# Optimization experiments

Hardware: AMD Instinct MI355X
Metric: run time of the kernel (lower is better)

Reference implementation:

```python
import jax, jax.numpy as jnp
import numpy as np

# dims
B, T, N, D, H, MRP = 16, 120, 24, 256, 8, 32
DP = D // H  # per-head depth = 32
NEG = -1e9


def setup_inputs() -> dict:
    key = jax.random.key(0)
    ks = jax.random.split(key, 32)
    g = lambda k, shape: jax.random.normal(k, shape, jnp.float32) * 0.02
    inp = {
        'x': jax.random.normal(ks[0], (B, T, N, D), jnp.float32),
        # causal look-ahead mask: 1 where attention is disallowed
        'mask': jnp.triu(jnp.ones((T, T), jnp.float32), 1),
        # per-joint temporal QKV (distinct Linear per joint, as in the per-joint ModuleList loops)
        'wq_t': g(ks[1], (N, D, D)), 'wk_t': g(ks[2], (N, D, D)), 'wv_t': g(ks[3], (N, D, D)),
        'bq_t': jnp.zeros((N, D), jnp.float32), 'bk_t': jnp.zeros((N, D), jnp.float32), 'bv_t': jnp.zeros((N, D), jnp.float32),
        'wo_t': g(ks[4], (D, D)), 'bo_t': jnp.zeros((D,), jnp.float32),
        # relative position key/value embedding tables [2*MRP+1, depth]
        'rel_key': g(ks[5], (2 * MRP + 1, DP)), 'rel_val': g(ks[6], (2 * MRP + 1, DP)),
        # spatial (across-joint) attention: shared linears
        'wq_s': g(ks[7], (D, D)), 'wk_s': g(ks[8], (D, D)), 'wv_s': g(ks[9], (D, D)), 'wo_s': g(ks[10], (D, D)),
        'bq_s': jnp.zeros((D,), jnp.float32), 'bk_s': jnp.zeros((D,), jnp.float32), 'bv_s': jnp.zeros((D,), jnp.float32), 'bo_s': jnp.zeros((D,), jnp.float32),
        # per-joint pointwise FFN
        'ff1_w': g(ks[11], (N, D, D)), 'ff1_b': jnp.zeros((N, D), jnp.float32),
        'ff2_w': g(ks[12], (N, D, D)), 'ff2_b': jnp.zeros((N, D), jnp.float32),
    }
    return inp


def _forward(x, mask, wq_t, wk_t, wv_t, bq_t, bk_t, bv_t, wo_t, bo_t,
             rel_key, rel_val, wq_s, wk_s, wv_s, wo_s, bq_s, bk_s, bv_s, bo_s,
             ff1_w, ff1_b, ff2_w, ff2_b):
    b, t, n, d = x.shape
    dp = d // H
    scale = 1.0 / jnp.sqrt(jnp.float32(dp))

    def joint_proj(y, w, bias):  # per-joint Linear: [b,t,n,d] x [n,d,e]
        return jnp.einsum('btnd,nde->btne', y, w) + bias

    def heads_t(y):  # -> [b, n, h, t, dp]
        return y.reshape(b, t, n, H, dp).transpose(0, 2, 3, 1, 4)

    # ---- temporal attention (per joint, with relative pos key/val embeddings) ----
    q = heads_t(joint_proj(x, wq_t, bq_t))
    k = heads_t(joint_proj(x, wk_t, bk_t))
    v = heads_t(joint_proj(x, wv_t, bv_t))
    rel_idx = jnp.clip(jnp.arange(t)[None, :] - jnp.arange(t)[:, None], -MRP, MRP) + MRP  # [t,t]
    rk = rel_key[rel_idx]   # [t,t,dp]
    rv = rel_val[rel_idx]   # [t,t,dp]
    logits = jnp.einsum('bnhtd,bnhsd->bnhts', q, k) + jnp.einsum('bnhtd,tsd->bnhts', q, rk)
    logits = logits * scale + mask * NEG
    attn = jax.nn.softmax(logits, axis=-1)
    out = jnp.einsum('bnhts,bnhsd->bnhtd', attn, v) + jnp.einsum('bnhts,tsd->bnhtd', attn, rv)
    out = out.transpose(0, 3, 1, 2, 4).reshape(b, t, n, d)
    t_out = jnp.einsum('btnd,de->btne', out, wo_t) + bo_t

    # ---- spatial attention (across joints at each timestep, shared linears) ----
    def heads_s(y):  # [b,t,n,d] -> [b,t,h,n,dp]
        return y.reshape(b, t, n, H, dp).transpose(0, 1, 3, 2, 4)

    qs = heads_s(jnp.einsum('btnd,de->btne', x, wq_s) + bq_s)
    ks_ = heads_s(jnp.einsum('btnd,de->btne', x, wk_s) + bk_s)
    vs = heads_s(jnp.einsum('btnd,de->btne', x, wv_s) + bv_s)
    s_logits = jnp.einsum('bthnd,bthmd->bthnm', qs, ks_) * scale
    s_attn = jax.nn.softmax(s_logits, axis=-1)
    s_out = jnp.einsum('bthnm,bthmd->bthnd', s_attn, vs)
    s_out = s_out.transpose(0, 1, 3, 2, 4).reshape(b, t, n, d)
    s_out = jnp.einsum('btnd,de->btne', s_out, wo_s) + bo_s

    # ---- parallel combination + residual ----
    y = x + t_out + s_out

    # ---- per-joint pointwise FFN + residual ----
    h = jax.nn.relu(joint_proj(y, ff1_w, ff1_b))
    ffn = joint_proj(h, ff2_w, ff2_b)
    return y + ffn


def reference(x, mask, wq_t, wk_t, wv_t, bq_t, bk_t, bv_t, wo_t, bo_t,
              rel_key, rel_val, wq_s, wk_s, wv_s, wo_s, bq_s, bk_s, bv_s, bo_s,
              ff1_w, ff1_b, ff2_w, ff2_b):
    return _forward(x, mask, wq_t, wk_t, wv_t, bq_t, bk_t, bv_t, wo_t, bo_t,
                    rel_key, rel_val, wq_s, wk_s, wv_s, wo_s, bq_s, bk_s, bv_s, bo_s,
                    ff1_w, ff1_b, ff2_w, ff2_b)
```

## Files before the change

kernel.cpp:

```cpp
#include <hip/hip_runtime.h>

#define B_    16
#define T_    120
#define N_    24
#define D_    256
#define H_    8
#define DP_   32
#define MRP_  32
#define BT_   (B_*T_)
#define M_    (B_*T_*N_)
#define TND   (N_*D_)
#define SCALE_ 0.17677669529663687f

typedef __attribute__((ext_vector_type(8))) short bf16x8;
typedef __attribute__((ext_vector_type(4))) float f32x4;

#define MEMBAR() asm volatile("" ::: "memory")

__device__ inline unsigned short f2bf(float f) {
    union { float f; unsigned u; } v; v.f = f;
    return (unsigned short)((v.u + 0x7FFF + ((v.u >> 16) & 1)) >> 16);
}
__device__ inline float bf2f(unsigned short u) {
    union { unsigned u; float f; } v; v.u = ((unsigned)u) << 16;
    return v.f;
}
__device__ __forceinline__ void gld16(const void* g, void* l) {
    __builtin_amdgcn_global_load_lds(
        (__attribute__((address_space(1))) void*)g,
        (__attribute__((address_space(3))) void*)l, 16, 0, 0);
}

__global__ __launch_bounds__(256) void convw(
    const float* __restrict__ wq_t, const float* __restrict__ wk_t,
    const float* __restrict__ wv_t, const float* __restrict__ wo_t,
    const float* __restrict__ wq_s, const float* __restrict__ wk_s,
    const float* __restrict__ wv_s, const float* __restrict__ wo_s,
    const float* __restrict__ ff1_w, const float* __restrict__ ff2_w,
    unsigned short* __restrict__ Wall)
{
    const int bx = blockIdx.x;
    const int m = bx >> 4, tile = bx & 15;
    const int d0 = (tile >> 2) * 64, e0 = (tile & 3) * 64;
    const float* src;
    if      (m < 24)  src = wq_t + (size_t)m * 65536;
    else if (m < 48)  src = wk_t + (size_t)(m-24) * 65536;
    else if (m < 72)  src = wv_t + (size_t)(m-48) * 65536;
    else if (m == 72) src = wo_t;
    else if (m == 73) src = wq_s;
    else if (m == 74) src = wk_s;
    else if (m == 75) src = wv_s;
    else if (m == 76) src = wo_s;
    else if (m < 101) src = ff1_w + (size_t)(m-77) * 65536;
    else              src = ff2_w + (size_t)(m-101) * 65536;
    unsigned short* dst = Wall + (size_t)m * 65536;

    __shared__ float t[64][65];
    const int tid = threadIdx.x;
#pragma unroll
    for (int i = 0; i < 4; ++i) {
        const int dr = (tid >> 4) + i*16;
        const int e4 = (tid & 15) * 4;
        const float4 v = *(const float4*)(src + (size_t)(d0+dr)*256 + e0 + e4);
        t[dr][e4] = v.x; t[dr][e4+1] = v.y; t[dr][e4+2] = v.z; t[dr][e4+3] = v.w;
    }
    __syncthreads();
#pragma unroll
    for (int i = 0; i < 2; ++i) {
        const int er = (tid >> 3) + i*32;
        const int c8 = (tid & 7) * 8;
        unsigned short tmp[8];
#pragma unroll
        for (int j = 0; j < 8; ++j) tmp[j] = f2bf(t[c8+j][er]);
        *(uint4*)&dst[(size_t)(e0+er)*256 + d0 + c8] = *(uint4*)tmp;
    }
}

__global__ __launch_bounds__(256) void convx(const float* __restrict__ x,
                                             unsigned short* __restrict__ xb)
{
    const size_t i = ((size_t)blockIdx.x*256 + threadIdx.x) * 8;
    const float4 a = *(const float4*)(x + i);
    const float4 b = *(const float4*)(x + i + 4);
    unsigned short tmp[8] = { f2bf(a.x), f2bf(a.y), f2bf(a.z), f2bf(a.w),
                              f2bf(b.x), f2bf(b.y), f2bf(b.z), f2bf(b.w) };
    *(uint4*)(xb + i) = *(uint4*)tmp;
}

__global__ __launch_bounds__(256) void convrel(
    const float* __restrict__ rel_key, const float* __restrict__ rel_val,
    unsigned short* __restrict__ relk_img, unsigned short* __restrict__ relv_img)
{
    const int tid = threadIdx.x;
    for (int i = tid; i < 48*32; i += 256) {
        const int c = i >> 5, d = i & 31;
        relk_img[i] = f2bf(rel_key[c*DP_ + d]);
    }
    for (int i = tid; i < 32*72; i += 256) {
        const int d = i / 72, c = i % 72;
        relv_img[i] = (c < 65) ? f2bf(rel_val[c*DP_ + d]) : (unsigned short)0;
    }
}

template<bool PJ>
__global__ __launch_bounds__(256, 6) void mgemm(
    const unsigned short* __restrict__ A, const unsigned short* __restrict__ Wt,
    const float* __restrict__ bias,
    const float* __restrict__ res1, const unsigned short* __restrict__ resb,
    float* __restrict__ outf, unsigned short* __restrict__ outb, int relu)
{
    __shared__ __align__(16) unsigned short As[2][64*32];
    __shared__ __align__(16) unsigned short Bs[2][64*32];
    const int tid  = threadIdx.x;
    const int wave = tid >> 6, lane = tid & 63;
    const int r16  = lane & 15, q4 = lane >> 4;

    const int qg  = (int)gridDim.x >> 3;
    const int wid = (blockIdx.x & 7) * qg + (blockIdx.x >> 3);
    const int rc  = wid >> 2, ec = wid & 3;

    size_t growbase; int rstride;
    const unsigned short* Wp; const float* bp;
    if (PJ) {
        const int n = rc / 30, tile = rc % 30;
        growbase = (size_t)(tile*64) * N_ + n; rstride = N_;
        Wp = Wt + (size_t)n * 65536; bp = bias + n * 256;
    } else {
        growbase = (size_t)rc * 64; rstride = 1;
        Wp = Wt; bp = bias;
    }
    const unsigned short* Wpe = Wp + (size_t)(ec*64) * 256;
    const int e0 = ec * 64;

    f32x4 acc[4];
#pragma unroll
    for (int i = 0; i < 4; ++i) acc[i] = (f32x4){0.f,0.f,0.f,0.f};

    const int arow = tid >> 2, ach = (tid & 3) * 8;

#define STAGE_(kc_, buf_) do {                                                  \
        const int k0_ = (kc_) * 32;                                             \
        gld16(A + (growbase + (size_t)arow*rstride)*256 + k0_ + ach,            \
              &As[buf_][wave*512]);                                             \
        gld16(Wpe + (size_t)arow*256 + k0_ + ach,                               \
              &Bs[buf_][wave*512]);                                             \
    } while (0)

    STAGE_(0, 0);
    STAGE_(1, 1);

#pragma unroll
    for (int kc = 0; kc < 8; ++kc) {
        const int cur = kc & 1;
        if (kc < 7) { asm volatile("s_waitcnt vmcnt(2)" ::: "memory"); }
        else        { asm volatile("s_waitcnt vmcnt(0)" ::: "memory"); }
        __builtin_amdgcn_sched_barrier(0);
        __builtin_amdgcn_s_barrier();

        const bf16x8 af = *(const bf16x8*)&As[cur][(wave*16 + r16)*32 + q4*8];
        bf16x8 bfr[4];
#pragma unroll
        for (int cs = 0; cs < 4; ++cs) bfr[cs] = *(const bf16x8*)&Bs[cur][(cs*16 + r16)*32 + q4*8];
#pragma unroll
        for (int cs = 0; cs < 4; ++cs)
            acc[cs] = __builtin_amdgcn_mfma_f32_16x16x32_bf16(af, bfr[cs], acc[cs], 0, 0, 0);

        __builtin_amdgcn_s_barrier();
        if (kc + 2 < 8) STAGE_(kc + 2, cur);
    }
#undef STAGE_

#pragma unroll
    for (int cs = 0; cs < 4; ++cs) {
        const int e = e0 + cs*16 + r16;
        const float bb = bp[e];
#pragma unroll
        for (int rg = 0; rg < 4; ++rg) {
            const int lr = wave*16 + q4*4 + rg;
            const size_t off = (growbase + (size_t)lr*rstride)*256 + e;
            float v = acc[cs][rg] + bb;
            if (relu) v = fmaxf(v, 0.f);
            if (res1) v += res1[off];
            if (resb) v += bf2f(resb[off]);
            if (outf) outf[off] = v;
            if (outb) outb[off] = f2bf(v);
        }
    }
}

template<bool PJ>
__global__ __launch_bounds__(256, 6) void mgemm_qkv(
    const unsigned short* __restrict__ A, const unsigned short* __restrict__ Wbase,
    const float* __restrict__ bq, const float* __restrict__ bk2,
    const float* __restrict__ bv,
    unsigned short* __restrict__ oq, unsigned short* __restrict__ ok2,
    unsigned short* __restrict__ ov)
{
    __shared__ __align__(16) unsigned short As[2][64*32];
    __shared__ __align__(16) unsigned short Bs[2][64*32];
    const int tid  = threadIdx.x;
    const int wave = tid >> 6, lane = tid & 63;
    const int r16  = lane & 15, q4 = lane >> 4;

    const int qg  = (int)gridDim.x >> 3;
    const int wid = (blockIdx.x & 7) * qg + (blockIdx.x >> 3);
    const int qkv = wid % 3;
    const int t2  = wid / 3;
    const int rc  = t2 >> 2, ec = t2 & 3;

    size_t growbase; int rstride;
    const unsigned short* Wp; const float* bp;
    if (PJ) {
        const int n = rc / 30, tile = rc % 30;
        growbase = (size_t)(tile*64) * N_ + n; rstride = N_;
        Wp = Wbase + ((size_t)qkv * 24 + n) * 65536;
        bp = (qkv == 0 ? bq : qkv == 1 ? bk2 : bv) + n * 256;
    } else {
        growbase = (size_t)rc * 64; rstride = 1;
        Wp = Wbase + (size_t)qkv * 65536;
        bp = (qkv == 0 ? bq : qkv == 1 ? bk2 : bv);
    }
    unsigned short* outp = (qkv == 0 ? oq : qkv == 1 ? ok2 : ov);
    const unsigned short* Wpe = Wp + (size_t)(ec*64) * 256;
    const int e0 = ec * 64;

    f32x4 acc[4];
#pragma unroll
    for (int i = 0; i < 4; ++i) acc[i] = (f32x4){0.f,0.f,0.f,0.f};

    const int arow = tid >> 2, ach = (tid & 3) * 8;

#define STAGE_(kc_, buf_) do {                                                  \
        const int k0_ = (kc_) * 32;                                             \
        gld16(A + (growbase + (size_t)arow*rstride)*256 + k0_ + ach,            \
              &As[buf_][wave*512]);                                             \
        gld16(Wpe + (size_t)arow*256 + k0_ + ach,                               \
              &Bs[buf_][wave*512]);                                             \
    } while (0)

    STAGE_(0, 0);
    STAGE_(1, 1);

#pragma unroll
    for (int kc = 0; kc < 8; ++kc) {
        const int cur = kc & 1;
        if (kc < 7) { asm volatile("s_waitcnt vmcnt(2)" ::: "memory"); }
        else        { asm volatile("s_waitcnt vmcnt(0)" ::: "memory"); }
        __builtin_amdgcn_sched_barrier(0);
        __builtin_amdgcn_s_barrier();

        const bf16x8 af = *(const bf16x8*)&As[cur][(wave*16 + r16)*32 + q4*8];
        bf16x8 bfr[4];
#pragma unroll
        for (int cs = 0; cs < 4; ++cs) bfr[cs] = *(const bf16x8*)&Bs[cur][(cs*16 + r16)*32 + q4*8];
#pragma unroll
        for (int cs = 0; cs < 4; ++cs)
            acc[cs] = __builtin_amdgcn_mfma_f32_16x16x32_bf16(af, bfr[cs], acc[cs], 0, 0, 0);

        __builtin_amdgcn_s_barrier();
        if (kc + 2 < 8) STAGE_(kc + 2, cur);
    }
#undef STAGE_

#pragma unroll
    for (int cs = 0; cs < 4; ++cs) {
        const int e = e0 + cs*16 + r16;
        const float bb = bp[e];
#pragma unroll
        for (int rg = 0; rg < 4; ++rg) {
            const int lr = wave*16 + q4*4 + rg;
            const size_t off = (growbase + (size_t)lr*rstride)*256 + e;
            outp[off] = f2bf(acc[cs][rg] + bb);
        }
    }
}

__global__ __launch_bounds__(256) void temporal_attn(
    const unsigned short* __restrict__ Q, const unsigned short* __restrict__ K,
    const unsigned short* __restrict__ V,
    const unsigned short* __restrict__ relk_img,
    const unsigned short* __restrict__ relv_img,
    unsigned short* __restrict__ out)
{
    __shared__ __align__(16) unsigned short ksb[128*32];
    __shared__ __align__(16) unsigned short vtb[32*136];
    __shared__ __align__(16) unsigned short rkb[48*32];
    __shared__ __align__(16) unsigned short rvtb[32*72];
    __shared__ __align__(16) unsigned short psb[4][16*136];
    __shared__ __align__(16) unsigned short awb[4][16*72];

    const int tid = threadIdx.x, wave = tid >> 6, lane = tid & 63;
    const int r = lane & 15, q4 = lane >> 4;
    const int wid = ((int)blockIdx.x & 7) * 384 + ((int)blockIdx.x >> 3);
    const int h = wid & 7;
    const int bn = wid >> 3;
    const int n = bn % N_;
    const int b = bn / N_;
    const size_t gb = ((size_t)(b*T_)*N_ + n)*D_ + h*DP_;

    {
        const int row0 = tid >> 2, ch0 = (tid & 3) * 8;
        gld16(K + gb + (size_t)row0*TND + ch0, ksb + (size_t)(wave*64)*8);
        int row1 = (256 + tid) >> 2; if (row1 > 119) row1 = 119;
        const int ch1 = ((256 + tid) & 3) * 8;
        gld16(K + gb + (size_t)row1*TND + ch1, ksb + (size_t)(256 + wave*64)*8);
    }
    bf16x8 aqs[2];
#pragma unroll
    for (int ti = 0; ti < 2; ++ti) {
        int qrow = (wave + ti*4)*16 + r; if (qrow > 119) qrow = 119;
        aqs[ti] = *(const bf16x8*)(Q + gb + (size_t)qrow*TND + q4*8);
    }
#pragma unroll
    for (int i = 0; i < 2; ++i) {
        const int slot = tid + i*256;
        if (slot < 480) {
            const int row = slot >> 2, ch = (slot & 3) * 8;
            union { uint4 u; unsigned short h8[8]; } vv;
            vv.u = *(const uint4*)(V + gb + (size_t)row*TND + ch);
#pragma unroll
            for (int j = 0; j < 8; ++j) vtb[(ch+j)*136 + row] = vv.h8[j];
        }
    }
    {
        const int row = tid >> 3, d2 = (tid & 7) * 2;
        *(unsigned*)&vtb[row*136 + 120 + d2] = 0u;
    }
    {
        const uint4* s1 = (const uint4*)relk_img;
        for (int i = tid; i < 192; i += 256) ((uint4*)rkb)[i] = s1[i];
        const uint4* s2 = (const uint4*)relv_img;
        for (int i = tid; i < 288; i += 256) ((uint4*)rvtb)[i] = s2[i];
    }
    __syncthreads();

    unsigned short* psbw = psb[wave];
    unsigned short* awbw = awb[wave];
    float* qrkp = (float*)psbw;

#pragma unroll
    for (int ti = 0; ti < 2; ++ti) {
        const int qt = wave + ti*4;
        const int t0 = qt * 16;
        const int stmax = ti ? 8 : 4;
        const int kcmax = ti ? 4 : 2;

        const bf16x8 aq = aqs[ti];
        __builtin_amdgcn_s_setprio(1);
        f32x4 lgacc[8];
#pragma unroll
        for (int st = 0; st < 8; ++st) {
            if (st < stmax) {
                const bf16x8 bk = *(const bf16x8*)&ksb[(st*16 + r)*32 + q4*8];
                lgacc[st] = __builtin_amdgcn_mfma_f32_16x16x32_bf16(aq, bk, (f32x4){0.f,0.f,0.f,0.f}, 0, 0, 0);
            }
        }
        f32x4 qr[3];
#pragma unroll
        for (int ck = 0; ck < 3; ++ck) {
            const bf16x8 bk = *(const bf16x8*)&rkb[(ck*16 + r)*32 + q4*8];
            qr[ck] = __builtin_amdgcn_mfma_f32_16x16x32_bf16(aq, bk, (f32x4){0.f,0.f,0.f,0.f}, 0, 0, 0);
        }
        __builtin_amdgcn_s_setprio(0);
#pragma unroll
        for (int ck = 0; ck < 3; ++ck)
#pragma unroll
            for (int rr = 0; rr < 4; ++rr)
                qrkp[(q4*4 + rr)*36 + ck*16 + r] = qr[ck][rr];
        MEMBAR();

        float p[4][8], far_[4];
#pragma unroll
        for (int rr = 0; rr < 4; ++rr) {
            const int row = q4*4 + rr;
            const int ta  = t0 + row;
            float v[8];
#pragma unroll
            for (int kt = 0; kt < 8; ++kt) {
                if (kt < stmax) {
                    const int s   = kt*16 + r;
                    const int idx = ta - s;
                    const int c   = (idx >= 32) ? 0 : (32 - idx);
                    const float qv = qrkp[row*36 + c];
                    v[kt] = (idx >= 0) ? (lgacc[kt][rr] + qv) * SCALE_ : -1e30f;
                }
            }
            float mx = v[0];
#pragma unroll
            for (int kt = 1; kt < 8; ++kt)
                if (kt < stmax) mx = fmaxf(mx, v[kt]);
#pragma unroll
            for (int off = 1; off < 16; off <<= 1) mx = fmaxf(mx, __shfl_xor(mx, off));
            float sum = 0.f;
#pragma unroll
            for (int kt = 0; kt < 8; ++kt)
                if (kt < stmax) { v[kt] = __expf(v[kt] - mx); sum += v[kt]; }
#pragma unroll
            for (int off = 1; off < 16; off <<= 1) sum += __shfl_xor(sum, off);
            const float inv = 1.f / sum;
            float fr = 0.f;
#pragma unroll
            for (int kt = 0; kt < 8; ++kt) {
                if (kt < stmax) {
                    p[rr][kt] = v[kt] * inv;
                    const int s = kt*16 + r;
                    if (ta - s >= 32) fr += p[rr][kt];
                }
            }
#pragma unroll
            for (int off = 1; off < 16; off <<= 1) fr += __shfl_xor(fr, off);
            far_[rr] = fr;
        }
        MEMBAR();

#pragma unroll
        for (int i = 0; i < 9; ++i) ((unsigned*)awbw)[lane + i*64] = 0u;
        MEMBAR();
#pragma unroll
        for (int rr = 0; rr < 4; ++rr) {
            const int row = q4*4 + rr;
            const int ta  = t0 + row;
#pragma unroll
            for (int kt = 0; kt < 8; ++kt) {
                if (kt < stmax) {
                    const int s = kt*16 + r;
                    psbw[row*136 + s] = f2bf(p[rr][kt]);
                    const int idx = ta - s;
                    if (idx >= 0 && idx < 32) awbw[row*72 + 32 - idx] = f2bf(p[rr][kt]);
                }
            }
            if (r == 0) awbw[row*72] = f2bf(far_[rr]);
        }
        MEMBAR();

#pragma unroll
        for (int ct = 0; ct < 2; ++ct) {
            f32x4 acc = {0.f, 0.f, 0.f, 0.f};
            __builtin_amdgcn_s_setprio(1);
#pragma unroll
            for (int kc = 0; kc < 4; ++kc) {
                if (kc < kcmax) {
                    const bf16x8 a  = *(const bf16x8*)&psbw[r*136 + kc*32 + q4*8];
                    const bf16x8 bb = *(const bf16x8*)&vtb[(ct*16 + r)*136 + kc*32 + q4*8];
                    acc = __builtin_amdgcn_mfma_f32_16x16x32_bf16(a, bb, acc, 0, 0, 0);
                }
            }
#pragma unroll
            for (int kc = 0; kc < 2; ++kc) {
                const bf16x8 a  = *(const bf16x8*)&awbw[r*72 + kc*32 + q4*8];
                const bf16x8 bb = *(const bf16x8*)&rvtb[(ct*16 + r)*72 + kc*32 + q4*8];
                acc = __builtin_amdgcn_mfma_f32_16x16x32_bf16(a, bb, acc, 0, 0, 0);
            }
            __builtin_amdgcn_s_setprio(0);
#pragma unroll
            for (int rr = 0; rr < 4; ++rr) {
                const int row = t0 + q4*4 + rr;
                if (row < 120)
                    out[gb + (size_t)row*TND + ct*16 + r] = f2bf(acc[rr]);
            }
        }
        MEMBAR();
    }
}

__global__ __launch_bounds__(512) void spatial_attn(
    const unsigned short* __restrict__ Qs, const unsigned short* __restrict__ Ks,
    const unsigned short* __restrict__ Vs, unsigned short* __restrict__ out)
{
    __shared__ __align__(16) unsigned short vt[256*40];
    __shared__ __align__(16) unsigned short pa[8][32*40];
    const int tid = threadIdx.x, wave = tid >> 6, lane = tid & 63;
    const int r16 = lane & 15, q4 = lane >> 4;
    const int h = wave;
    const size_t base = (size_t)blockIdx.x * N_ * D_;

    bf16x8 kf[2], qf[2];
#pragma unroll
    for (int t = 0; t < 2; ++t) {
        int row = t*16 + r16; if (row > 23) row = 23;
        kf[t] = *(const bf16x8*)(Ks + base + (size_t)row*D_ + h*DP_ + q4*8);
        qf[t] = *(const bf16x8*)(Qs + base + (size_t)row*D_ + h*DP_ + q4*8);
    }

    for (int slot = tid; slot < 768; slot += 512) {
        const int m = slot >> 5, ec = slot & 31;
        union { uint4 u; unsigned short s_[8]; } vv;
        vv.u = *(const uint4*)(Vs + base + (size_t)m*D_ + ec*8);
#pragma unroll
        for (int j = 0; j < 8; ++j) vt[(ec*8 + j)*40 + m] = vv.s_[j];
    }
    for (int z = tid; z < 256*4; z += 512)
        *(unsigned*)&vt[(z >> 2)*40 + 24 + (z & 3)*2] = 0u;
    __syncthreads();

    f32x4 st[2][2];
#pragma unroll
    for (int it = 0; it < 2; ++it)
#pragma unroll
        for (int mt = 0; mt < 2; ++mt)
            st[mt][it] = __builtin_amdgcn_mfma_f32_16x16x32_bf16(
                kf[mt], qf[it], (f32x4){0.f,0.f,0.f,0.f}, 0, 0, 0);

    unsigned short* paw = pa[wave];
#pragma unroll
    for (int it = 0; it < 2; ++it) {
        float v[2][4];
#pragma unroll
        for (int mt = 0; mt < 2; ++mt)
#pragma unroll
            for (int rg = 0; rg < 4; ++rg) {
                const int m = mt*16 + q4*4 + rg;
                v[mt][rg] = (m < 24) ? st[mt][it][rg] * SCALE_ : -1e30f;
            }
        float mx = v[0][0];
#pragma unroll
        for (int mt = 0; mt < 2; ++mt)
#pragma unroll
            for (int rg = 0; rg < 4; ++rg) mx = fmaxf(mx, v[mt][rg]);
        mx = fmaxf(mx, __shfl_xor(mx, 16));
        mx = fmaxf(mx, __shfl_xor(mx, 32));
        float sum = 0.f;
#pragma unroll
        for (int mt = 0; mt < 2; ++mt)
#pragma unroll
            for (int rg = 0; rg < 4; ++rg) { v[mt][rg] = __expf(v[mt][rg] - mx); sum += v[mt][rg]; }
        sum += __shfl_xor(sum, 16);
        sum += __shfl_xor(sum, 32);
        const float inv = 1.f / sum;
#pragma unroll
        for (int mt = 0; mt < 2; ++mt) {
            unsigned short p4[4];
#pragma unroll
            for (int rg = 0; rg < 4; ++rg) p4[rg] = f2bf(v[mt][rg] * inv);
            *(uint2*)&paw[(it*16 + r16)*40 + mt*16 + q4*4] = *(uint2*)p4;
        }
    }
    MEMBAR();

    bf16x8 ap[2], bv[2];
#pragma unroll
    for (int t = 0; t < 2; ++t) {
        ap[t] = *(const bf16x8*)&paw[(t*16 + r16)*40 + q4*8];
        bv[t] = *(const bf16x8*)&vt[(h*DP_ + t*16 + r16)*40 + q4*8];
    }
#pragma unroll
    for (int it = 0; it < 2; ++it)
#pragma unroll
        for (int ct = 0; ct < 2; ++ct) {
            const f32x4 o = __builtin_amdgcn_mfma_f32_16x16x32_bf16(
                ap[it], bv[ct], (f32x4){0.f,0.f,0.f,0.f}, 0, 0, 0);
#pragma unroll
            for (int rg = 0; rg < 4; ++rg) {
                const int i = it*16 + q4*4 + rg;
                if (i < 24)
                    out[base + (size_t)i*D_ + h*DP_ + ct*16 + r16] = f2bf(o[rg]);
            }
        }
}

extern "C" void kernel_launch(void* const* d_in, const int* in_sizes, int n_in,
                              void* d_out, int out_size, void* d_ws, size_t ws_size,
                              hipStream_t stream) {
    const float* x       = (const float*)d_in[0];
    const float* wq_t    = (const float*)d_in[2];
    const float* wk_t    = (const float*)d_in[3];
    const float* wv_t    = (const float*)d_in[4];
    const float* bq_t    = (const float*)d_in[5];
    const float* bk_t    = (const float*)d_in[6];
    const float* bv_t    = (const float*)d_in[7];
    const float* wo_t    = (const float*)d_in[8];
    const float* bo_t    = (const float*)d_in[9];
    const float* rel_key = (const float*)d_in[10];
    const float* rel_val = (const float*)d_in[11];
    const float* wq_s    = (const float*)d_in[12];
    const float* wk_s    = (const float*)d_in[13];
    const float* wv_s    = (const float*)d_in[14];
    const float* wo_s    = (const float*)d_in[15];
    const float* bq_s    = (const float*)d_in[16];
    const float* bk_s    = (const float*)d_in[17];
    const float* bv_s    = (const float*)d_in[18];
    const float* bo_s    = (const float*)d_in[19];
    const float* ff1_w   = (const float*)d_in[20];
    const float* ff1_b   = (const float*)d_in[21];
    const float* ff2_w   = (const float*)d_in[22];
    const float* ff2_b   = (const float*)d_in[23];

    float* out = (float*)d_out;
    unsigned short* outbf = (unsigned short*)d_out;
    unsigned short* ws = (unsigned short*)d_ws;
    const size_t WSZ = (size_t)125 * 65536;
    const size_t SZ  = (size_t)M_ * D_;
    unsigned short* Wall = ws;
    unsigned short* xbf  = Wall + WSZ;
    unsigned short* bufA = xbf + SZ;
    unsigned short* bufB = bufA + SZ;
    unsigned short* bufC = bufB + SZ;
    unsigned short* relk = bufC + SZ;
    unsigned short* relv = relk + 1536;

    const dim3 blk(256);

    convw<<<dim3(125*16), blk, 0, stream>>>(wq_t, wk_t, wv_t, wo_t, wq_s, wk_s, wv_s, wo_s, ff1_w, ff2_w, Wall);
    convx<<<dim3(5760), blk, 0, stream>>>(x, xbf);
    convrel<<<dim3(1), blk, 0, stream>>>(rel_key, rel_val, relk, relv);

    mgemm_qkv<true ><<<dim3(8640), blk, 0, stream>>>(xbf, Wall, bq_t, bk_t, bv_t, bufA, bufB, bufC);
    temporal_attn<<<dim3(B_*N_*H_), blk, 0, stream>>>(bufA, bufB, bufC, relk, relv, bufA);
    mgemm<false><<<dim3(2880), blk, 0, stream>>>(bufA, Wall + 72ull*65536, bo_t, nullptr, nullptr, nullptr, outbf, 0);
    mgemm_qkv<false><<<dim3(8640), blk, 0, stream>>>(xbf, Wall + 73ull*65536, bq_s, bk_s, bv_s, bufB, bufC, bufA);
    spatial_attn<<<dim3(BT_), dim3(512), 0, stream>>>(bufB, bufC, bufA, bufB);
    mgemm<false><<<dim3(2880), blk, 0, stream>>>(bufB, Wall + 76ull*65536, bo_s, x, outbf, nullptr, bufC, 0);
    mgemm<true ><<<dim3(2880), blk, 0, stream>>>(bufC, Wall + 77ull*65536, ff1_b, nullptr, nullptr, nullptr, bufA, 1);
    mgemm<true ><<<dim3(2880), blk, 0, stream>>>(bufA, Wall + 101ull*65536, ff2_b, nullptr, bufC, out, nullptr, 0);
}
```

Measured before the change: 443.0 us.

## Fuse conversion kernels and merge both output projections into one concatenated-K GEMM

```diff
diff --git a/kernel.cpp b/kernel.cpp
--- a/kernel.cpp
+++ b/kernel.cpp
@@ -31,74 +31,69 @@
         (__attribute__((address_space(3))) void*)l, 16, 0, 0);
 }
 
-__global__ __launch_bounds__(256) void convw(
+__global__ __launch_bounds__(256) void convall(
     const float* __restrict__ wq_t, const float* __restrict__ wk_t,
     const float* __restrict__ wv_t, const float* __restrict__ wo_t,
     const float* __restrict__ wq_s, const float* __restrict__ wk_s,
     const float* __restrict__ wv_s, const float* __restrict__ wo_s,
     const float* __restrict__ ff1_w, const float* __restrict__ ff2_w,
-    unsigned short* __restrict__ Wall)
-{
-    const int bx = blockIdx.x;
-    const int m = bx >> 4, tile = bx & 15;
-    const int d0 = (tile >> 2) * 64, e0 = (tile & 3) * 64;
-    const float* src;
-    if      (m < 24)  src = wq_t + (size_t)m * 65536;
-    else if (m < 48)  src = wk_t + (size_t)(m-24) * 65536;
-    else if (m < 72)  src = wv_t + (size_t)(m-48) * 65536;
-    else if (m == 72) src = wo_t;
-    else if (m == 73) src = wq_s;
-    else if (m == 74) src = wk_s;
-    else if (m == 75) src = wv_s;
-    else if (m == 76) src = wo_s;
-    else if (m < 101) src = ff1_w + (size_t)(m-77) * 65536;
-    else              src = ff2_w + (size_t)(m-101) * 65536;
-    unsigned short* dst = Wall + (size_t)m * 65536;
-
-    __shared__ float t[64][65];
-    const int tid = threadIdx.x;
-#pragma unroll
-    for (int i = 0; i < 4; ++i) {
-        const int dr = (tid >> 4) + i*16;
-        const int e4 = (tid & 15) * 4;
-        const float4 v = *(const float4*)(src + (size_t)(d0+dr)*256 + e0 + e4);
-        t[dr][e4] = v.x; t[dr][e4+1] = v.y; t[dr][e4+2] = v.z; t[dr][e4+3] = v.w;
-    }
-    __syncthreads();
-#pragma unroll
-    for (int i = 0; i < 2; ++i) {
-        const int er = (tid >> 3) + i*32;
-        const int c8 = (tid & 7) * 8;
-        unsigned short tmp[8];
-#pragma unroll
-        for (int j = 0; j < 8; ++j) tmp[j] = f2bf(t[c8+j][er]);
-        *(uint4*)&dst[(size_t)(e0+er)*256 + d0 + c8] = *(uint4*)tmp;
-    }
-}
-
-__global__ __launch_bounds__(256) void convx(const float* __restrict__ x,
-                                             unsigned short* __restrict__ xb)
-{
-    const size_t i = ((size_t)blockIdx.x*256 + threadIdx.x) * 8;
-    const float4 a = *(const float4*)(x + i);
-    const float4 b = *(const float4*)(x + i + 4);
-    unsigned short tmp[8] = { f2bf(a.x), f2bf(a.y), f2bf(a.z), f2bf(a.w),
-                              f2bf(b.x), f2bf(b.y), f2bf(b.z), f2bf(b.w) };
-    *(uint4*)(xb + i) = *(uint4*)tmp;
-}
-
-__global__ __launch_bounds__(256) void convrel(
-    const float* __restrict__ rel_key, const float* __restrict__ rel_val,
+    const float* __restrict__ x, const float* __restrict__ rel_key,
+    const float* __restrict__ rel_val,
+    unsigned short* __restrict__ Wall, unsigned short* __restrict__ xb,
     unsigned short* __restrict__ relk_img, unsigned short* __restrict__ relv_img)
 {
-    const int tid = threadIdx.x;
-    for (int i = tid; i < 48*32; i += 256) {
-        const int c = i >> 5, d = i & 31;
-        relk_img[i] = f2bf(rel_key[c*DP_ + d]);
-    }
-    for (int i = tid; i < 32*72; i += 256) {
-        const int d = i / 72, c = i % 72;
-        relv_img[i] = (c < 65) ? f2bf(rel_val[c*DP_ + d]) : (unsigned short)0;
+    __shared__ float t[64][65];
+    const int bx = blockIdx.x, tid = threadIdx.x;
+
+    if (bx < 2000) {
+        const int m = bx >> 4, tile = bx & 15;
+        const int d0 = (tile >> 2) * 64, e0 = (tile & 3) * 64;
+        const float* src;
+        if      (m < 24)  src = wq_t + (size_t)m * 65536;
+        else if (m < 48)  src = wk_t + (size_t)(m-24) * 65536;
+        else if (m < 72)  src = wv_t + (size_t)(m-48) * 65536;
+        else if (m == 72) src = wo_t;
+        else if (m == 73) src = wq_s;
+        else if (m == 74) src = wk_s;
+        else if (m == 75) src = wv_s;
+        else if (m == 76) src = wo_s;
+        else if (m < 101) src = ff1_w + (size_t)(m-77) * 65536;
+        else              src = ff2_w + (size_t)(m-101) * 65536;
+        unsigned short* dst = Wall + (size_t)m * 65536;
+
+#pragma unroll
+        for (int i = 0; i < 4; ++i) {
+            const int dr = (tid >> 4) + i*16;
+            const int e4 = (tid & 15) * 4;
+            const float4 v = *(const float4*)(src + (size_t)(d0+dr)*256 + e0 + e4);
+            t[dr][e4] = v.x; t[dr][e4+1] = v.y; t[dr][e4+2] = v.z; t[dr][e4+3] = v.w;
+        }
+        __syncthreads();
+#pragma unroll
+        for (int i = 0; i < 2; ++i) {
+            const int er = (tid >> 3) + i*32;
+            const int c8 = (tid & 7) * 8;
+            unsigned short tmp[8];
+#pragma unroll
+            for (int j = 0; j < 8; ++j) tmp[j] = f2bf(t[c8+j][er]);
+            *(uint4*)&dst[(size_t)(e0+er)*256 + d0 + c8] = *(uint4*)tmp;
+        }
+    } else if (bx < 7760) {
+        const size_t i = ((size_t)(bx - 2000)*256 + tid) * 8;
+        const float4 a = *(const float4*)(x + i);
+        const float4 b = *(const float4*)(x + i + 4);
+        unsigned short tmp[8] = { f2bf(a.x), f2bf(a.y), f2bf(a.z), f2bf(a.w),
+                                  f2bf(b.x), f2bf(b.y), f2bf(b.z), f2bf(b.w) };
+        *(uint4*)(xb + i) = *(uint4*)tmp;
+    } else {
+        for (int i = tid; i < 48*32; i += 256) {
+            const int c = i >> 5, d = i & 31;
+            relk_img[i] = f2bf(rel_key[c*DP_ + d]);
+        }
+        for (int i = tid; i < 32*72; i += 256) {
+            const int d = i / 72, c = i % 72;
+            relv_img[i] = (c < 65) ? f2bf(rel_val[c*DP_ + d]) : (unsigned short)0;
+        }
     }
 }
 
@@ -271,6 +266,83 @@
             const int lr = wave*16 + q4*4 + rg;
             const size_t off = (growbase + (size_t)lr*rstride)*256 + e;
             outp[off] = f2bf(acc[cs][rg] + bb);
+        }
+    }
+}
+
+__global__ __launch_bounds__(256, 6) void mgemm_wo(
+    const unsigned short* __restrict__ A1, const unsigned short* __restrict__ W1,
+    const unsigned short* __restrict__ A2, const unsigned short* __restrict__ W2,
+    const float* __restrict__ b1, const float* __restrict__ b2,
+    const float* __restrict__ resx, unsigned short* __restrict__ outb)
+{
+    __shared__ __align__(16) unsigned short As[2][64*32];
+    __shared__ __align__(16) unsigned short Bs[2][64*32];
+    const int tid  = threadIdx.x;
+    const int wave = tid >> 6, lane = tid & 63;
+    const int r16  = lane & 15, q4 = lane >> 4;
+
+    const int qg  = (int)gridDim.x >> 3;
+    const int wid = (blockIdx.x & 7) * qg + (blockIdx.x >> 3);
+    const int rc  = wid >> 2, ec = wid & 3;
+
+    const size_t growbase = (size_t)rc * 64;
+    const unsigned short* W1e = W1 + (size_t)(ec*64) * 256;
+    const unsigned short* W2e = W2 + (size_t)(ec*64) * 256;
+    const int e0 = ec * 64;
+
+    f32x4 acc[4];
+#pragma unroll
+    for (int i = 0; i < 4; ++i) acc[i] = (f32x4){0.f,0.f,0.f,0.f};
+
+    const int arow = tid >> 2, ach = (tid & 3) * 8;
+
+#define STG_(Ap_, Wp_, kc_, buf_) do {                                          \
+        const int k0_ = (kc_) * 32;                                             \
+        gld16((Ap_) + (growbase + (size_t)arow)*256 + k0_ + ach,                \
+              &As[buf_][wave*512]);                                             \
+        gld16((Wp_) + (size_t)arow*256 + k0_ + ach,                             \
+              &Bs[buf_][wave*512]);                                             \
+    } while (0)
+
+    STG_(A1, W1e, 0, 0);
+    STG_(A1, W1e, 1, 1);
+
+#pragma unroll
+    for (int s = 0; s < 16; ++s) {
+        const int cur = s & 1;
+        if (s < 15) { asm volatile("s_waitcnt vmcnt(2)" ::: "memory"); }
+        else        { asm volatile("s_waitcnt vmcnt(0)" ::: "memory"); }
+        __builtin_amdgcn_sched_barrier(0);
+        __builtin_amdgcn_s_barrier();
+
+        const bf16x8 af = *(const bf16x8*)&As[cur][(wave*16 + r16)*32 + q4*8];
+        bf16x8 bfr[4];
+#pragma unroll
+        for (int cs = 0; cs < 4; ++cs) bfr[cs] = *(const bf16x8*)&Bs[cur][(cs*16 + r16)*32 + q4*8];
+#pragma unroll
+        for (int cs = 0; cs < 4; ++cs)
+            acc[cs] = __builtin_amdgcn_mfma_f32_16x16x32_bf16(af, bfr[cs], acc[cs], 0, 0, 0);
+
+        __builtin_amdgcn_s_barrier();
+        if (s + 2 < 16) {
+            const int ns = s + 2;
+            const unsigned short* Ap = (ns < 8) ? A1 : A2;
+            const unsigned short* Wp = (ns < 8) ? W1e : W2e;
+            STG_(Ap, Wp, ns & 7, cur);
+        }
+    }
+#undef STG_
+
+#pragma unroll
+    for (int cs = 0; cs < 4; ++cs) {
+        const int e = e0 + cs*16 + r16;
+        const float bb = b1[e] + b2[e];
+#pragma unroll
+        for (int rg = 0; rg < 4; ++rg) {
+            const int lr = wave*16 + q4*4 + rg;
+            const size_t off = (growbase + (size_t)lr)*256 + e;
+            outb[off] = f2bf(acc[cs][rg] + bb + resx[off]);
         }
     }
 }
@@ -600,16 +672,17 @@
 
     const dim3 blk(256);
 
-    convw<<<dim3(125*16), blk, 0, stream>>>(wq_t, wk_t, wv_t, wo_t, wq_s, wk_s, wv_s, wo_s, ff1_w, ff2_w, Wall);
-    convx<<<dim3(5760), blk, 0, stream>>>(x, xbf);
-    convrel<<<dim3(1), blk, 0, stream>>>(rel_key, rel_val, relk, relv);
+    convall<<<dim3(7761), blk, 0, stream>>>(wq_t, wk_t, wv_t, wo_t, wq_s, wk_s, wv_s, wo_s,
+                                            ff1_w, ff2_w, x, rel_key, rel_val,
+                                            Wall, xbf, relk, relv);
 
     mgemm_qkv<true ><<<dim3(8640), blk, 0, stream>>>(xbf, Wall, bq_t, bk_t, bv_t, bufA, bufB, bufC);
     temporal_attn<<<dim3(B_*N_*H_), blk, 0, stream>>>(bufA, bufB, bufC, relk, relv, bufA);
-    mgemm<false><<<dim3(2880), blk, 0, stream>>>(bufA, Wall + 72ull*65536, bo_t, nullptr, nullptr, nullptr, outbf, 0);
-    mgemm_qkv<false><<<dim3(8640), blk, 0, stream>>>(xbf, Wall + 73ull*65536, bq_s, bk_s, bv_s, bufB, bufC, bufA);
-    spatial_attn<<<dim3(BT_), dim3(512), 0, stream>>>(bufB, bufC, bufA, bufB);
-    mgemm<false><<<dim3(2880), blk, 0, stream>>>(bufB, Wall + 76ull*65536, bo_s, x, outbf, nullptr, bufC, 0);
+    mgemm_qkv<false><<<dim3(8640), blk, 0, stream>>>(xbf, Wall + 73ull*65536, bq_s, bk_s, bv_s, bufB, bufC, outbf);
+    spatial_attn<<<dim3(BT_), dim3(512), 0, stream>>>(bufB, bufC, outbf, bufB);
+    mgemm_wo<<<dim3(2880), blk, 0, stream>>>(bufA, Wall + 72ull*65536,
+                                             bufB, Wall + 76ull*65536,
+                                             bo_t, bo_s, x, bufC);
     mgemm<true ><<<dim3(2880), blk, 0, stream>>>(bufC, Wall + 77ull*65536, ff1_b, nullptr, nullptr, nullptr, bufA, 1);
     mgemm<true ><<<dim3(2880), blk, 0, stream>>>(bufA, Wall + 101ull*65536, ff2_b, nullptr, bufC, out, nullptr, 0);
 }
```

Result: faster. 411.6 us (-7.1%).
